# Kernel tuning notes

Measured on AMD Instinct MI355X. Metric: run time of the kernel, lower is better.

The kernel has to match this reference:

```python
import jax, jax.numpy as jnp
import numpy as np

H_DIM = 1152
N_HEADS = 12
HEAD_DIM = H_DIM // N_HEADS  # 96, divisible by 3
SCALE_ROT = 32 // 16  # character_pixel_size // patch_size


def setup_inputs() -> dict:
    key = jax.random.key(0)
    ks = jax.random.split(key, 9)
    std = 1.0 / np.sqrt(H_DIM)
    return {
        "hidden_states": jax.random.normal(ks[0], (8, 1025, H_DIM), dtype=jnp.float32),
        "Wq": jax.random.normal(ks[1], (H_DIM, H_DIM), dtype=jnp.float32) * std,
        "bq": jax.random.normal(ks[2], (H_DIM,), dtype=jnp.float32) * 0.02,
        "Wk": jax.random.normal(ks[3], (H_DIM, H_DIM), dtype=jnp.float32) * std,
        "bk": jax.random.normal(ks[4], (H_DIM,), dtype=jnp.float32) * 0.02,
        "Wv": jax.random.normal(ks[5], (H_DIM, H_DIM), dtype=jnp.float32) * std,
        "bv": jax.random.normal(ks[6], (H_DIM,), dtype=jnp.float32) * 0.02,
        "Wo": jax.random.normal(ks[7], (H_DIM, H_DIM), dtype=jnp.float32) * std,
        "bo": jax.random.normal(ks[8], (H_DIM,), dtype=jnp.float32) * 0.02,
        "rows": 32,
        "cols": 32,
    }


def _rotary_tables(seq_len, rows, cols, dtype):
    # (seq_len, n_triplets) trig tables based on 2-D patch grid position
    inv_freq = 1.0 / (10000.0 ** (jnp.arange(0, HEAD_DIM, 3, dtype=dtype) / (HEAD_DIM * SCALE_ROT)))
    ids = jnp.arange(seq_len)
    cls_offset = 1 if seq_len != rows * cols else 0
    grid_ids = jnp.clip(ids - cls_offset, 0)
    row_ids = (grid_ids // cols).astype(dtype)
    col_ids = (grid_ids % cols).astype(dtype)
    theta = row_ids[:, None] * inv_freq
    psi = col_ids[:, None] * inv_freq
    return jnp.cos(theta), jnp.sin(theta), jnp.cos(psi), jnp.sin(psi)


def _apply_rotary_3d(x, ct, st, cp, sp):
    # x: (b, s, h, d) -> view as (b, s, h, t, 3)
    b, s, h, d = x.shape
    x = x.reshape(b, s, h, d // 3, 3)
    ct = ct[None, :, None, :]
    st = st[None, :, None, :]
    cp = cp[None, :, None, :]
    sp = sp[None, :, None, :]
    x0, x1, x2 = x[..., 0], x[..., 1], x[..., 2]
    r0 = cp * x0 + sp * st * x1 + sp * ct * x2
    r1 = ct * x1 - st * x2
    r2 = -sp * x0 + cp * st * x1 + cp * ct * x2
    return jnp.stack((r0, r1, r2), axis=-1).reshape(b, s, h, d)


def reference(hidden_states, Wq, bq, Wk, bk, Wv, bv, Wo, bo, rows, cols):
    b, s, _ = hidden_states.shape
    dtype = hidden_states.dtype
    scale = HEAD_DIM ** -0.5

    q = (hidden_states @ Wq + bq).reshape(b, s, N_HEADS, HEAD_DIM)
    k = (hidden_states @ Wk + bk).reshape(b, s, N_HEADS, HEAD_DIM)
    v = (hidden_states @ Wv + bv).reshape(b, s, N_HEADS, HEAD_DIM)

    ct, st, cp, sp = _rotary_tables(s, rows, cols, dtype)
    q = _apply_rotary_3d(q, ct, st, cp, sp)
    k = _apply_rotary_3d(k, ct, st, cp, sp)

    # (b, h, s, s) attention scores
    scores = jnp.einsum("bqhd,bkhd->bhqk", q, k) * scale
    probs = jax.nn.softmax(scores.astype(jnp.float32), axis=-1).astype(dtype)
    ctx = jnp.einsum("bhqk,bkhd->bqhd", probs, v).reshape(b, s, H_DIM)
    out = ctx @ Wo + bo
    return out
```

## Files before the change

kernel.cpp:

```cpp
#include <hip/hip_runtime.h>
#include <stdint.h>

#define BATCH 8
#define SEQ   1025
#define HDIM  1152
#define NH    12
#define DH    96
#define MROWS (BATCH*SEQ)
#define N_QKV (3*HDIM)
#define KD    HDIM
#define NT2   18

typedef __attribute__((ext_vector_type(8))) short short8;
typedef __attribute__((ext_vector_type(4))) short short4_;
typedef __attribute__((ext_vector_type(4))) float float4_;
typedef __attribute__((ext_vector_type(16))) float f32x16;

#define AS1 __attribute__((address_space(1)))
#define AS3 __attribute__((address_space(3)))
#define BARM() do { asm volatile("" ::: "memory"); __builtin_amdgcn_s_barrier(); asm volatile("" ::: "memory"); } while (0)

__device__ inline float bf2f(short s) {
  union { unsigned u; float f; } x; x.u = ((unsigned)(unsigned short)s) << 16; return x.f;
}
__device__ inline short f2bf(float f) {
  union { float f; unsigned u; } x; x.f = f;
  unsigned r = (x.u + 0x7fffu + ((x.u >> 16) & 1u)) >> 16;
  return (short)r;
}

__global__ __launch_bounds__(256) void convx(const float* __restrict__ hs, short* __restrict__ X) {
  int i = blockIdx.x * 256 + threadIdx.x;
  float4_ v = ((const float4_*)hs)[i];
  short4_ o;
  o[0] = f2bf(v[0]); o[1] = f2bf(v[1]); o[2] = f2bf(v[2]); o[3] = f2bf(v[3]);
  ((short4_*)X)[i] = o;
}

__global__ __launch_bounds__(256) void convw_t(const float* __restrict__ W0,
                                               const float* __restrict__ W1,
                                               const float* __restrict__ W2,
                                               short* __restrict__ Wt) {
  __shared__ float T[64][65];
  const int z = blockIdx.z;
  const float* W = z == 0 ? W0 : (z == 1 ? W1 : W2);
  const int n0 = blockIdx.x * 64, k0 = blockIdx.y * 64;
  const int tid = threadIdx.x;
  const int r = tid >> 2, cq = (tid & 3) * 16;
#pragma unroll
  for (int u = 0; u < 4; ++u) {
    float4_ v = *(const float4_*)&W[(long)(k0 + r) * HDIM + n0 + cq + u * 4];
    T[r][cq + u * 4 + 0] = v[0]; T[r][cq + u * 4 + 1] = v[1];
    T[r][cq + u * 4 + 2] = v[2]; T[r][cq + u * 4 + 3] = v[3];
  }
  __syncthreads();
  const int n = tid >> 2, kq = (tid & 3) * 16;
  short out[16];
#pragma unroll
  for (int u = 0; u < 16; ++u) out[u] = f2bf(T[kq + u][n]);
  short* dst = Wt + (long)(z * HDIM + n0 + n) * KD + k0 + kq;
  *(short8*)dst = *(short8*)&out[0];
  *(short8*)(dst + 8) = *(short8*)&out[8];
}

template<int OUTF32>
__global__ __launch_bounds__(512, 2) void gemm256(
    const short* __restrict__ A, const short* __restrict__ Bt,
    const float* __restrict__ b0, const float* __restrict__ b1, const float* __restrict__ b2,
    void* __restrict__ Cout, const int N, const int MT) {
  __shared__ alignas(16) short Lds[65536];
  const int tid = threadIdx.x;
  const int l = tid & 63, w = tid >> 6;
  const int lrow = l & 15, lg = l >> 4;
  const int wr = w >> 2, wc = w & 3;

  const int nwg = gridDim.x;
  const int qq = nwg >> 3, r8 = nwg & 7;
  const int xcd = blockIdx.x & 7, loc = blockIdx.x >> 3;
  const int wg = (xcd < r8 ? xcd * (qq + 1) : r8 * (qq + 1) + (xcd - r8) * qq) + loc;
  const int mt = wg % MT, nt = wg / MT;
  const int m0 = mt * 256, n0 = nt * 256;

#define KEYR(r) ((((r) & 3)) ^ (((r) >> 2) & 3))

  const short* asrc[2]; const short* bsrc[2];
#pragma unroll
  for (int i = 0; i < 2; ++i) {
    int p = i * 512 + tid;
    int row = p >> 2;
    int lslot = (p & 3) ^ KEYR(row);
    int ra = m0 + row; if (ra > MROWS - 1) ra = MROWS - 1;
    int rb = n0 + row; if (rb > N - 1) rb = N - 1;
    asrc[i] = A + (long)ra * KD + lslot * 8;
    bsrc[i] = Bt + (long)rb * KD + lslot * 8;
  }

#define STAGEA(sb, kh, kt_, i) \
  __builtin_amdgcn_global_load_lds((const AS1 void*)(asrc[i] + (kt_) * 64 + (kh) * 32), \
      (AS3 void*)(&Lds[(sb) * 16384 + (kh) * 8192 + (i * 512 + tid) * 8]), 16, 0, 0)
#define STAGEB(sb, kh, kt_, i) \
  __builtin_amdgcn_global_load_lds((const AS1 void*)(bsrc[i] + (kt_) * 64 + (kh) * 32), \
      (AS3 void*)(&Lds[32768 + (sb) * 16384 + (kh) * 8192 + (i * 512 + tid) * 8]), 16, 0, 0)
#define LDA(dst, base, mi) { const int row_ = wr * 128 + (mi) * 16 + lrow; \
  dst = *(const short8*)&Lds[(base) + row_ * 32 + ((lg ^ KEYR(row_)) << 3)]; }
#define LDB(dst, base, nj) { const int row_ = wc * 64 + (nj) * 16 + lrow; \
  dst = *(const short8*)&Lds[(base) + row_ * 32 + ((lg ^ KEYR(row_)) << 3)]; }
#define MFMA16(a, b, c) __builtin_amdgcn_mfma_f32_16x16x32_bf16(a, b, c, 0, 0, 0)
#define MF16(mb, A0, A1, A2, A3) \
  acc[(mb)+0][0] = MFMA16(A0, bf0, acc[(mb)+0][0]); \
  acc[(mb)+0][1] = MFMA16(A0, bf1, acc[(mb)+0][1]); \
  acc[(mb)+0][2] = MFMA16(A0, bf2, acc[(mb)+0][2]); \
  acc[(mb)+0][3] = MFMA16(A0, bf3, acc[(mb)+0][3]); \
  acc[(mb)+1][0] = MFMA16(A1, bf0, acc[(mb)+1][0]); \
  acc[(mb)+1][1] = MFMA16(A1, bf1, acc[(mb)+1][1]); \
  acc[(mb)+1][2] = MFMA16(A1, bf2, acc[(mb)+1][2]); \
  acc[(mb)+1][3] = MFMA16(A1, bf3, acc[(mb)+1][3]); \
  acc[(mb)+2][0] = MFMA16(A2, bf0, acc[(mb)+2][0]); \
  acc[(mb)+2][1] = MFMA16(A2, bf1, acc[(mb)+2][1]); \
  acc[(mb)+2][2] = MFMA16(A2, bf2, acc[(mb)+2][2]); \
  acc[(mb)+2][3] = MFMA16(A2, bf3, acc[(mb)+2][3]); \
  acc[(mb)+3][0] = MFMA16(A3, bf0, acc[(mb)+3][0]); \
  acc[(mb)+3][1] = MFMA16(A3, bf1, acc[(mb)+3][1]); \
  acc[(mb)+3][2] = MFMA16(A3, bf2, acc[(mb)+3][2]); \
  acc[(mb)+3][3] = MFMA16(A3, bf3, acc[(mb)+3][3]);

  float4_ acc[8][4];
#pragma unroll
  for (int mi = 0; mi < 8; ++mi)
#pragma unroll
    for (int nj = 0; nj < 4; ++nj) acc[mi][nj] = (float4_)(0.f);

  STAGEA(0, 0, 0, 0); STAGEA(0, 0, 0, 1);
  STAGEB(0, 0, 0, 0); STAGEB(0, 0, 0, 1);
  STAGEA(0, 1, 0, 0); STAGEA(0, 1, 0, 1);
  STAGEB(0, 1, 0, 0); STAGEB(0, 1, 0, 1);
  asm volatile("s_waitcnt vmcnt(4)" ::: "memory");
  BARM();

  for (int kt = 0; kt < NT2; ++kt) {
    const int cb = kt & 1, sb = (kt + 1) & 1;
    const bool dost = (kt + 1) < NT2;
    const int aK0 = cb * 16384, aK1 = aK0 + 8192;
    const int bK0 = 32768 + cb * 16384, bK1 = bK0 + 8192;
    short8 af0, af1, af2, af3, bf0, bf1, bf2, bf3;

    if (dost) { STAGEA(sb, 0, kt + 1, 0); STAGEA(sb, 0, kt + 1, 1); }
    LDB(bf0, bK0, 0); LDB(bf1, bK0, 1); LDB(bf2, bK0, 2); LDB(bf3, bK0, 3);
    LDA(af0, aK0, 0); LDA(af1, aK0, 1); LDA(af2, aK0, 2); LDA(af3, aK0, 3);
    __builtin_amdgcn_s_setprio(1);
    MF16(0, af0, af1, af2, af3);
    __builtin_amdgcn_s_setprio(0);
    if (dost) { STAGEB(sb, 0, kt + 1, 0); STAGEB(sb, 0, kt + 1, 1); }
    LDA(af0, aK0, 4); LDA(af1, aK0, 5); LDA(af2, aK0, 6); LDA(af3, aK0, 7);
    __builtin_amdgcn_s_setprio(1);
    MF16(4, af0, af1, af2, af3);
    __builtin_amdgcn_s_setprio(0);
    if (dost) asm volatile("s_waitcnt vmcnt(4)" ::: "memory");
    else      asm volatile("s_waitcnt vmcnt(0)" ::: "memory");
    BARM();
    if (dost) { STAGEA(sb, 1, kt + 1, 0); STAGEA(sb, 1, kt + 1, 1); }
    LDB(bf0, bK1, 0); LDB(bf1, bK1, 1); LDB(bf2, bK1, 2); LDB(bf3, bK1, 3);
    LDA(af0, aK1, 0); LDA(af1, aK1, 1); LDA(af2, aK1, 2); LDA(af3, aK1, 3);
    __builtin_amdgcn_s_setprio(1);
    MF16(0, af0, af1, af2, af3);
    __builtin_amdgcn_s_setprio(0);
    if (dost) { STAGEB(sb, 1, kt + 1, 0); STAGEB(sb, 1, kt + 1, 1); }
    LDA(af0, aK1, 4); LDA(af1, aK1, 5); LDA(af2, aK1, 6); LDA(af3, aK1, 7);
    __builtin_amdgcn_s_setprio(1);
    MF16(4, af0, af1, af2, af3);
    __builtin_amdgcn_s_setprio(0);
    asm volatile("s_waitcnt lgkmcnt(0)" ::: "memory");
    asm volatile("s_waitcnt vmcnt(4)" ::: "memory");
    BARM();
  }

  float bias[4];
#pragma unroll
  for (int nj = 0; nj < 4; ++nj) {
    int cn = n0 + wc * 64 + nj * 16 + lrow;
    float bv_ = 0.f;
    if (cn < N) bv_ = (N == HDIM) ? b0[cn]
                                  : (cn < HDIM ? b0[cn] : (cn < 2 * HDIM ? b1[cn - HDIM] : b2[cn - 2 * HDIM]));
    bias[nj] = bv_;
  }
#pragma unroll
  for (int mi = 0; mi < 8; ++mi)
#pragma unroll
    for (int r = 0; r < 4; ++r) {
      int m = m0 + wr * 128 + mi * 16 + lg * 4 + r;
      if (m >= MROWS) continue;
#pragma unroll
      for (int nj = 0; nj < 4; ++nj) {
        int cn = n0 + wc * 64 + nj * 16 + lrow;
        if (cn >= N) continue;
        float v = acc[mi][nj][r] + bias[nj];
        if (OUTF32) ((float*)Cout)[(long)m * N + cn] = v;
        else        ((short*)Cout)[(long)m * N + cn] = f2bf(v);
      }
    }
#undef STAGEA
#undef STAGEB
#undef LDA
#undef LDB
#undef MFMA16
#undef MF16
#undef KEYR
}

__global__ __launch_bounds__(256) void rotary_q(short* __restrict__ QKV,
                                                const int* __restrict__ rowsp,
                                                const int* __restrict__ colsp) {
  int idx = blockIdx.x * 256 + threadIdx.x;
  if (idx >= MROWS * NH * 4) return;
  const int qt = idx & 3;
  const int hm = idx >> 2;
  const int h = hm % NH, m = hm / NH;
  const int s = m % SEQ;
  const int cols = colsp[0], rws = rowsp[0];
  const int off = (SEQ != rws * cols) ? 1 : 0;
  int gid = s - off; if (gid < 0) gid = 0;
  const float frow = (float)(gid / cols), fcol = (float)(gid % cols);
  union { short sh[24]; short8 v[3]; } u;
  short* p = QKV + (long)m * N_QKV + h * DH + qt * 24;
  u.v[0] = *(short8*)p; u.v[1] = *(short8*)(p + 8); u.v[2] = *(short8*)(p + 16);
#pragma unroll
  for (int t = 0; t < 8; ++t) {
    int j = qt * 8 + t;
    float invf = exp2f((float)(3 * j) * (-13.287712379549449f / 192.0f));
    float st, ct, sp, cp;
    __sincosf(frow * invf, &st, &ct);
    __sincosf(fcol * invf, &sp, &cp);
    float x0 = bf2f(u.sh[3 * t]), x1 = bf2f(u.sh[3 * t + 1]), x2 = bf2f(u.sh[3 * t + 2]);
    u.sh[3 * t]     = f2bf( cp * x0 + sp * st * x1 + sp * ct * x2);
    u.sh[3 * t + 1] = f2bf( ct * x1 - st * x2);
    u.sh[3 * t + 2] = f2bf(-sp * x0 + cp * st * x1 + cp * ct * x2);
  }
  *(short8*)p = u.v[0]; *(short8*)(p + 8) = u.v[1]; *(short8*)(p + 16) = u.v[2];
}

__global__ __launch_bounds__(256) void fragpack(const short* __restrict__ QKV,
                                                short* __restrict__ Kf,
                                                short* __restrict__ Vf,
                                                const int* __restrict__ rowsp,
                                                const int* __restrict__ colsp) {
  __shared__ short L[64 * 96];
  const int t = blockIdx.x, bh = blockIdx.y;
  const int b = bh / NH, h = bh % NH;
  const int tid = threadIdx.x;
#pragma unroll
  for (int i = 0; i < 3; ++i) {
    int cc = i * 256 + tid;
    int kv = cc / 384;
    int rm = cc % 384;
    int r = rm / 12, m = rm % 12;
    int s = t * 32 + r; if (s > SEQ - 1) s = SEQ - 1;
    const short* src = QKV + (long)(b * SEQ + s) * N_QKV + (kv ? 2 * HDIM : HDIM) + h * DH + m * 8;
    *(short8*)&L[cc * 8] = *(const short8*)src;
  }
  __syncthreads();
  {
    const int cols = colsp[0], rws = rowsp[0];
    const int off = (SEQ != rws * cols) ? 1 : 0;
#pragma unroll
    for (int i = 0; i < 4; ++i) {
      int idx2 = i * 256 + tid;
      int r = idx2 >> 5, j = idx2 & 31;
      int s = t * 32 + r; if (s > SEQ - 1) s = SEQ - 1;
      int gid = s - off; if (gid < 0) gid = 0;
      float invf = exp2f((float)(3 * j) * (-13.287712379549449f / 192.0f));
      float st, ct, sp, cp;
      __sincosf((float)(gid / cols) * invf, &st, &ct);
      __sincosf((float)(gid % cols) * invf, &sp, &cp);
      short* pp = &L[r * 96 + 3 * j];
      float x0 = bf2f(pp[0]), x1 = bf2f(pp[1]), x2 = bf2f(pp[2]);
      pp[0] = f2bf( cp * x0 + sp * st * x1 + sp * ct * x2);
      pp[1] = f2bf( ct * x1 - st * x2);
      pp[2] = f2bf(-sp * x0 + cp * st * x1 + cp * ct * x2);
    }
  }
  __syncthreads();
#pragma unroll
  for (int i = 0; i < 3; ++i) {
    int oc = i * 256 + tid;
    if (oc < 384) {
      int c = oc / 64, ll = oc & 63;
      int qi = ll & 31, hi = ll >> 5;
      short8 v = *(const short8*)&L[qi * 96 + c * 16 + hi * 8];
      *(short8*)(Kf + (((long)(bh * 33 + t) * 6 + c) * 64 + ll) * 8) = v;
    } else {
      int oc2 = oc - 384;
      int d = oc2 / 128, sl = (oc2 / 64) & 1, ll = oc2 & 63;
      int qi = ll & 31, hi = ll >> 5;
      short8 v;
#pragma unroll
      for (int j = 0; j < 8; ++j)
        v[j] = L[32 * 96 + (sl * 16 + hi * 8 + j) * 96 + d * 32 + qi];
      *(short8*)(Vf + ((((long)(bh * 33 + t) * 3 + d) * 2 + sl) * 64 + ll) * 8) = v;
    }
  }
}

__global__ __launch_bounds__(128, 3) void attn_kernel(const short* __restrict__ QKV,
                                                      const short* __restrict__ Kf,
                                                      const short* __restrict__ Vf,
                                                      short* __restrict__ CTX) {
  const int tid = threadIdx.x;
  const int l = tid & 63, w = tid >> 6;
  const int qi = l & 31, hi = l >> 5;
  const int bid = blockIdx.x;
  const int xcd = bid & 7, jj = bid >> 3;
  const int bh = xcd * 12 + jj / 17;
  const int qb = jj % 17;
  const int b = bh / NH, h = bh % NH;
  const int s = qb * 64 + w * 32 + qi;
  const int sq = s > SEQ - 1 ? SEQ - 1 : s;

  const float scale = 0.1020620726159658f;
  const short* Qr = QKV + (long)(b * SEQ + sq) * N_QKV + h * DH;
  short8 qf[6];
#pragma unroll
  for (int c = 0; c < 6; ++c) {
    short8 v = *(const short8*)(Qr + c * 16 + hi * 8);
#pragma unroll
    for (int j = 0; j < 8; ++j) v[j] = f2bf(bf2f(v[j]) * scale);
    qf[c] = v;
  }

  const short* Kb = Kf + (long)bh * 33 * 6 * 64 * 8;
  const short* Vb = Vf + (long)bh * 33 * 6 * 64 * 8;

  f32x16 ctxv[3];
#pragma unroll
  for (int d = 0; d < 3; ++d) ctxv[d] = (f32x16)(0.f);
  float m_ = -1e30f, l_ = 0.f;

  for (int t = 0; t < 33; ++t) {
    f32x16 S = (f32x16)(0.f);
#pragma unroll
    for (int c = 0; c < 6; ++c) {
      short8 kf = *(const short8*)(Kb + (((long)t * 6 + c) * 64 + l) * 8);
      S = __builtin_amdgcn_mfma_f32_32x32x16_bf16(kf, qf[c], S, 0, 0, 0);
    }
    if (t == 32) {
      S[0] = hi ? -1e30f : S[0];
#pragma unroll
      for (int r = 1; r < 16; ++r) S[r] = -1e30f;
    }
    float tm = S[0];
#pragma unroll
    for (int r = 1; r < 16; ++r) tm = fmaxf(tm, S[r]);
    tm = fmaxf(tm, __shfl_xor(tm, 32));
    if (!__all(tm - m_ <= 8.f)) {
      float mn = fmaxf(m_, tm);
      float alpha = __expf(m_ - mn);
      m_ = mn;
      l_ *= alpha;
#pragma unroll
      for (int d = 0; d < 3; ++d)
#pragma unroll
        for (int r = 0; r < 16; ++r) ctxv[d][r] *= alpha;
    }
    float ts = 0.f;
#pragma unroll
    for (int r = 0; r < 16; ++r) { float p = __expf(S[r] - m_); S[r] = p; ts += p; }
    ts += __shfl_xor(ts, 32);
    l_ += ts;

    unsigned pk_[8];
#pragma unroll
    for (int j = 0; j < 8; ++j)
      pk_[j] = (unsigned)(unsigned short)f2bf(S[2 * j]) |
               ((unsigned)(unsigned short)f2bf(S[2 * j + 1]) << 16);
    unsigned s0 = hi ? pk_[0] : pk_[2];
    unsigned s1 = hi ? pk_[1] : pk_[3];
    unsigned s2 = hi ? pk_[4] : pk_[6];
    unsigned s3 = hi ? pk_[5] : pk_[7];
    unsigned r0 = __shfl_xor(s0, 32);
    unsigned r1 = __shfl_xor(s1, 32);
    unsigned r2 = __shfl_xor(s2, 32);
    unsigned r3 = __shfl_xor(s3, 32);
    union PF { unsigned u[4]; short8 s8; } f0, f1;
    f0.u[0] = hi ? r0 : pk_[0];
    f0.u[1] = hi ? r1 : pk_[1];
    f0.u[2] = hi ? pk_[2] : r0;
    f0.u[3] = hi ? pk_[3] : r1;
    f1.u[0] = hi ? r2 : pk_[4];
    f1.u[1] = hi ? r3 : pk_[5];
    f1.u[2] = hi ? pk_[6] : r2;
    f1.u[3] = hi ? pk_[7] : r3;

#pragma unroll
    for (int d = 0; d < 3; ++d) {
      const short* Vr = Vb + (((long)t * 3 + d) * 2 * 64) * 8;
      short8 vf0 = *(const short8*)(Vr + l * 8);
      ctxv[d] = __builtin_amdgcn_mfma_f32_32x32x16_bf16(vf0, f0.s8, ctxv[d], 0, 0, 0);
      short8 vf1 = *(const short8*)(Vr + (64 + l) * 8);
      ctxv[d] = __builtin_amdgcn_mfma_f32_32x32x16_bf16(vf1, f1.s8, ctxv[d], 0, 0, 0);
    }
  }

  float invl = 1.f / l_;
  if (s <= SEQ - 1) {
    short* Cr = CTX + (long)(b * SEQ + s) * HDIM + h * DH;
#pragma unroll
    for (int d = 0; d < 3; ++d)
#pragma unroll
      for (int g = 0; g < 4; ++g) {
        short4_ o;
#pragma unroll
        for (int r = 0; r < 4; ++r) o[r] = f2bf(ctxv[d][4 * g + r] * invl);
        *(short4_*)(Cr + d * 32 + 8 * g + 4 * hi) = o;
      }
  }
}

extern "C" void kernel_launch(void* const* d_in, const int* in_sizes, int n_in,
                              void* d_out, int out_size, void* d_ws, size_t ws_size,
                              hipStream_t stream) {
  const float* hs = (const float*)d_in[0];
  const float* Wq = (const float*)d_in[1];
  const float* bq = (const float*)d_in[2];
  const float* Wk = (const float*)d_in[3];
  const float* bk = (const float*)d_in[4];
  const float* Wv = (const float*)d_in[5];
  const float* bv = (const float*)d_in[6];
  const float* Wo = (const float*)d_in[7];
  const float* bo = (const float*)d_in[8];
  const int* rows = (const int*)d_in[9];
  const int* cols = (const int*)d_in[10];
  float* out = (float*)d_out;

  char* ws = (char*)d_ws;
  short* X   = (short*)(ws);
  short* Wt  = (short*)(ws + 18892800);
  short* Wot = (short*)(ws + 26855424);
  short* QKV = (short*)(ws + 29509632);
  short* Vf  = (short*)(ws + 86188032);
  short* CTX = (short*)(ws + 105652224);
  short* Kf  = (short*)(ws);

  convx<<<9225, 256, 0, stream>>>(hs, X);
  convw_t<<<dim3(18, 18, 3), 256, 0, stream>>>(Wq, Wk, Wv, Wt);
  convw_t<<<dim3(18, 18, 1), 256, 0, stream>>>(Wo, Wo, Wo, Wot);
  gemm256<0><<<462, 512, 0, stream>>>(X, Wt, bq, bk, bv, QKV, N_QKV, 33);
  rotary_q<<<1538, 256, 0, stream>>>(QKV, rows, cols);
  fragpack<<<dim3(33, 96), 256, 0, stream>>>(QKV, Kf, Vf, rows, cols);
  attn_kernel<<<1632, 128, 0, stream>>>(QKV, Kf, Vf, CTX);
  gemm256<1><<<165, 512, 0, stream>>>(CTX, Wot, bo, bo, bo, out, HDIM, 33);
}
```

Baseline: 279.2 us.

## Change GEMM LDS swizzle to paired-row XOR and add barrier-phased load/MFMA scheduling

Replaces the 4-slot LDS XOR swizzle with an 8-slot scheme that packs two rows per 64-element line, aiming to reduce LDS bank conflicts on the ds_read of A/B fragments. It also reorders each k-half so LDS fragment reads are issued before the next global_load_lds staging, then adds extra workgroup barriers and lgkmcnt(0) waits with sched_barrier around each MFMA block. The extra barriers synchronize waves into phases, which could serialize work and add stalls.

```diff
diff --git a/kernel.cpp b/kernel.cpp
--- a/kernel.cpp
+++ b/kernel.cpp
@@ -19,6 +19,7 @@
 #define AS1 __attribute__((address_space(1)))
 #define AS3 __attribute__((address_space(3)))
 #define BARM() do { asm volatile("" ::: "memory"); __builtin_amdgcn_s_barrier(); asm volatile("" ::: "memory"); } while (0)
+#define LGKM0() do { asm volatile("s_waitcnt lgkmcnt(0)" ::: "memory"); __builtin_amdgcn_sched_barrier(0); } while (0)
 
 __device__ inline float bf2f(short s) {
   union { unsigned u; float f; } x; x.u = ((unsigned)(unsigned short)s) << 16; return x.f;
@@ -81,18 +82,17 @@
   const int mt = wg % MT, nt = wg / MT;
   const int m0 = mt * 256, n0 = nt * 256;
 
-#define KEYR(r) ((((r) & 3)) ^ (((r) >> 2) & 3))
-
   const short* asrc[2]; const short* bsrc[2];
 #pragma unroll
   for (int i = 0; i < 2; ++i) {
     int p = i * 512 + tid;
-    int row = p >> 2;
-    int lslot = (p & 3) ^ KEYR(row);
+    int wl = (p & 7) ^ ((p >> 3) & 7);
+    int row = ((p >> 3) << 1) | (wl >> 2);
+    int kc = (wl & 3) * 8;
     int ra = m0 + row; if (ra > MROWS - 1) ra = MROWS - 1;
     int rb = n0 + row; if (rb > N - 1) rb = N - 1;
-    asrc[i] = A + (long)ra * KD + lslot * 8;
-    bsrc[i] = Bt + (long)rb * KD + lslot * 8;
+    asrc[i] = A + (long)ra * KD + kc;
+    bsrc[i] = Bt + (long)rb * KD + kc;
   }
 
 #define STAGEA(sb, kh, kt_, i) \
@@ -102,9 +102,11 @@
   __builtin_amdgcn_global_load_lds((const AS1 void*)(bsrc[i] + (kt_) * 64 + (kh) * 32), \
       (AS3 void*)(&Lds[32768 + (sb) * 16384 + (kh) * 8192 + (i * 512 + tid) * 8]), 16, 0, 0)
 #define LDA(dst, base, mi) { const int row_ = wr * 128 + (mi) * 16 + lrow; \
-  dst = *(const short8*)&Lds[(base) + row_ * 32 + ((lg ^ KEYR(row_)) << 3)]; }
+  dst = *(const short8*)&Lds[(base) + ((row_ >> 1) << 6) + \
+      (((((row_ & 1) << 2) + lg) ^ ((row_ >> 1) & 7)) << 3)]; }
 #define LDB(dst, base, nj) { const int row_ = wc * 64 + (nj) * 16 + lrow; \
-  dst = *(const short8*)&Lds[(base) + row_ * 32 + ((lg ^ KEYR(row_)) << 3)]; }
+  dst = *(const short8*)&Lds[(base) + ((row_ >> 1) << 6) + \
+      (((((row_ & 1) << 2) + lg) ^ ((row_ >> 1) & 7)) << 3)]; }
 #define MFMA16(a, b, c) __builtin_amdgcn_mfma_f32_16x16x32_bf16(a, b, c, 0, 0, 0)
 #define MF16(mb, A0, A1, A2, A3) \
   acc[(mb)+0][0] = MFMA16(A0, bf0, acc[(mb)+0][0]); \
@@ -144,33 +146,42 @@
     const int bK0 = 32768 + cb * 16384, bK1 = bK0 + 8192;
     short8 af0, af1, af2, af3, bf0, bf1, bf2, bf3;
 
-    if (dost) { STAGEA(sb, 0, kt + 1, 0); STAGEA(sb, 0, kt + 1, 1); }
     LDB(bf0, bK0, 0); LDB(bf1, bK0, 1); LDB(bf2, bK0, 2); LDB(bf3, bK0, 3);
     LDA(af0, aK0, 0); LDA(af1, aK0, 1); LDA(af2, aK0, 2); LDA(af3, aK0, 3);
+    if (dost) { STAGEA(sb, 0, kt + 1, 0); STAGEA(sb, 0, kt + 1, 1); }
+    BARM();
+    LGKM0();
     __builtin_amdgcn_s_setprio(1);
     MF16(0, af0, af1, af2, af3);
     __builtin_amdgcn_s_setprio(0);
+    BARM();
+    LDA(af0, aK0, 4); LDA(af1, aK0, 5); LDA(af2, aK0, 6); LDA(af3, aK0, 7);
     if (dost) { STAGEB(sb, 0, kt + 1, 0); STAGEB(sb, 0, kt + 1, 1); }
-    LDA(af0, aK0, 4); LDA(af1, aK0, 5); LDA(af2, aK0, 6); LDA(af3, aK0, 7);
+    BARM();
+    LGKM0();
     __builtin_amdgcn_s_setprio(1);
     MF16(4, af0, af1, af2, af3);
     __builtin_amdgcn_s_setprio(0);
     if (dost) asm volatile("s_waitcnt vmcnt(4)" ::: "memory");
     else      asm volatile("s_waitcnt vmcnt(0)" ::: "memory");
     BARM();
-    if (dost) { STAGEA(sb, 1, kt + 1, 0); STAGEA(sb, 1, kt + 1, 1); }
     LDB(bf0, bK1, 0); LDB(bf1, bK1, 1); LDB(bf2, bK1, 2); LDB(bf3, bK1, 3);
     LDA(af0, aK1, 0); LDA(af1, aK1, 1); LDA(af2, aK1, 2); LDA(af3, aK1, 3);
+    if (dost) { STAGEA(sb, 1, kt + 1, 0); STAGEA(sb, 1, kt + 1, 1); }
+    BARM();
+    LGKM0();
     __builtin_amdgcn_s_setprio(1);
     MF16(0, af0, af1, af2, af3);
     __builtin_amdgcn_s_setprio(0);
+    BARM();
+    LDA(af0, aK1, 4); LDA(af1, aK1, 5); LDA(af2, aK1, 6); LDA(af3, aK1, 7);
     if (dost) { STAGEB(sb, 1, kt + 1, 0); STAGEB(sb, 1, kt + 1, 1); }
-    LDA(af0, aK1, 4); LDA(af1, aK1, 5); LDA(af2, aK1, 6); LDA(af3, aK1, 7);
+    BARM();
+    LGKM0();
     __builtin_amdgcn_s_setprio(1);
     MF16(4, af0, af1, af2, af3);
     __builtin_amdgcn_s_setprio(0);
-    asm volatile("s_waitcnt lgkmcnt(0)" ::: "memory");
-    asm volatile("s_waitcnt vmcnt(4)" ::: "memory");
+    if (dost) asm volatile("s_waitcnt vmcnt(4)" ::: "memory");
     BARM();
   }
 
@@ -204,7 +215,6 @@
 #undef LDB
 #undef MFMA16
 #undef MF16
-#undef KEYR
 }
 
 __global__ __launch_bounds__(256) void rotary_q(short* __restrict__ QKV,
```

New measurement: 275.3 us. Within noise of the previous version (-1.4%).
